# Kernel optimization log

Hardware: AMD Instinct MI355X
Metric: run time of the kernel (lower is better)

Reference implementation:

```python
import jax, jax.numpy as jnp
import numpy as np

B, C, HID, H, W = 4, 256, 128, 64, 64

def setup_inputs() -> dict:
    key = jax.random.key(0)
    k0, k1, k2, k3, k4 = jax.random.split(key, 5)
    x = jax.random.normal(k0, (B, C, H, W), dtype=jnp.float32)
    # 1x1 conv weights, no bias: [out_ch, in_ch]
    s_in = 1.0 / np.sqrt(C)
    s_hid = 1.0 / np.sqrt(HID)
    w_theta = jax.random.uniform(k1, (HID, C), jnp.float32, -s_in, s_in)
    w_phi = jax.random.uniform(k2, (HID, C), jnp.float32, -s_in, s_in)
    w_g = jax.random.uniform(k3, (HID, C), jnp.float32, -s_in, s_in)
    w_mask = jax.random.uniform(k4, (C, HID), jnp.float32, -s_hid, s_hid)
    return {"x": x, "w_theta": w_theta, "w_phi": w_phi, "w_g": w_g, "w_mask": w_mask}

def reference(x, w_theta, w_phi, w_g, w_mask):
    b, c, h, w = x.shape
    n = h * w
    xf = x.reshape(b, c, n)                      # [B,C,N]
    theta = jnp.einsum('oc,bcn->bno', w_theta, xf)  # [B,N,hid]
    phi = jnp.einsum('oc,bcn->bon', w_phi, xf)      # [B,hid,N]
    g = jnp.einsum('oc,bcn->bno', w_g, xf)          # [B,N,hid]
    scores = jnp.einsum('bnk,bkm->bnm', theta, phi)  # [B,N,N], no scale
    attn = jax.nn.softmax(scores, axis=1)            # unconventional axis=1
    out = jnp.einsum('bnm,bmo->bno', attn, g)        # [B,N,hid]
    mask = jnp.einsum('co,bno->bcn', w_mask, out).reshape(b, c, h, w)
    return x + mask
```

## Files before the change

### kernel.cpp

```cpp
#include <hip/hip_runtime.h>

#define BB 4
#define CC 256
#define HIDD 128
#define NN 4096

typedef short s8v __attribute__((ext_vector_type(8)));
typedef _Float16 h8v __attribute__((ext_vector_type(8)));
typedef float f4v __attribute__((ext_vector_type(4)));
typedef unsigned int u4v __attribute__((ext_vector_type(4)));
typedef unsigned short u16b;

static __device__ __forceinline__ float b2f(unsigned short u) {
    union { unsigned int i; float f; } v; v.i = ((unsigned int)u) << 16; return v.f;
}
static __device__ __forceinline__ unsigned short f2b(float f) {
    union { float f; unsigned int i; } v; v.f = f;
    unsigned int i = v.i;
    return (unsigned short)((i + 0x7fffu + ((i >> 16) & 1u)) >> 16);
}
static __device__ __forceinline__ u16b f2h_bits(float f) {
    union { _Float16 h; u16b u; } v; v.h = (_Float16)f; return v.u;
}
static __device__ __forceinline__ unsigned int cvt_pk_bf16(float lo, float hi) {
    unsigned int r;
    asm("v_cvt_pk_bf16_f32 %0, %1, %2" : "=v"(r) : "v"(lo), "v"(hi));
    return r;
}

__device__ __forceinline__ int swz(int k, int rc, int CB) {
    return (((k >> 5) * CB + (rc >> 4)) * 64 + ((k >> 3) & 3) * 16 + (rc & 15)) * 8 + (k & 7);
}
__device__ __forceinline__ int gswz(int m, int o) {
    int kb = m >> 5, mm = m & 31;
    int qs = (mm >> 2) & 3;
    int js = ((mm >> 4) & 1) * 4 + (mm & 3);
    return ((kb * 8 + (o >> 4)) * 64 + qs * 16 + (o & 15)) * 8 + js;
}

__global__ __launch_bounds__(256) void prep_kernel(
    const float* __restrict__ wt, const float* __restrict__ wp,
    const float* __restrict__ wg, const float* __restrict__ wm,
    u16b* __restrict__ wF, u16b* __restrict__ wmB)
{
    int t = blockIdx.x * 256 + threadIdx.x;
    wF[t]         = f2h_bits(wt[t]);
    wF[32768 + t] = f2h_bits(wp[t]);
    wF[65536 + t] = f2h_bits(wg[t]);
    wmB[t]        = f2b(wm[t]);
}

__global__ __launch_bounds__(256) void proj_kernel(
    const float* __restrict__ x, const u16b* __restrict__ wF,
    u16b* __restrict__ thetaF, u16b* __restrict__ phiF, u16b* __restrict__ gB)
{
    int wave = blockIdx.x * 4 + (threadIdx.x >> 6);
    int lane = threadIdx.x & 63;
    int l15 = lane & 15, q = lane >> 4;
    int b = wave >> 9;
    int rem = wave & 511;
    int ntile = rem >> 1;
    int half = rem & 1;
    int n0 = ntile << 4;
    const float* xb = x + (size_t)b * CC * NN;

    f4v acc[3][4];
#pragma unroll
    for (int m = 0; m < 3; m++)
#pragma unroll
        for (int i = 0; i < 4; i++) acc[m][i] = (f4v){0.f, 0.f, 0.f, 0.f};

    float xv[8];
    {
        const float* xp = xb + (size_t)(q * 8) * NN + n0 + l15;
#pragma unroll
        for (int j = 0; j < 8; j++) xv[j] = xp[(size_t)j * NN];
    }

    for (int kc = 0; kc < 8; kc++) {
        int c0 = kc * 32;
        float xn[8];
        if (kc < 7) {
            const float* xp = xb + (size_t)(c0 + 32 + q * 8) * NN + n0 + l15;
#pragma unroll
            for (int j = 0; j < 8; j++) xn[j] = xp[(size_t)j * NN];
        }
        h8v bx;
#pragma unroll
        for (int j = 0; j < 8; j++) bx[j] = (_Float16)xv[j];
#pragma unroll
        for (int mat = 0; mat < 3; mat++) {
#pragma unroll
            for (int otl = 0; otl < 4; otl++) {
                int ot = half * 4 + otl;
                const h8v* ap = reinterpret_cast<const h8v*>(
                    wF + mat * 32768 + (ot * 16 + l15) * CC + c0 + q * 8);
                acc[mat][otl] = __builtin_amdgcn_mfma_f32_16x16x32_f16(*ap, bx, acc[mat][otl], 0, 0, 0);
            }
        }
        if (kc < 7) {
#pragma unroll
            for (int j = 0; j < 8; j++) xv[j] = xn[j];
        }
    }

    size_t boff = (size_t)b * (NN * HIDD);
#pragma unroll
    for (int otl = 0; otl < 4; otl++) {
#pragma unroll
        for (int r = 0; r < 4; r++) {
            int o = (half * 4 + otl) * 16 + q * 4 + r;
            int n = n0 + l15;
            int offTP = swz(o, n, NN / 16);
            thetaF[boff + offTP] = f2h_bits(acc[0][otl][r]);
            phiF[boff + offTP]   = f2h_bits(acc[1][otl][r]);
            gB[boff + gswz(n, o)] = f2b(acc[2][otl][r]);
        }
    }
}

__global__ __launch_bounds__(256, 2) void stats_kernel(
    const u16b* __restrict__ thetaF, const u16b* __restrict__ phiF,
    float* __restrict__ Lraw)
{
    int xcd = blockIdx.x & 7;
    int inner = blockIdx.x >> 3;
    int b = xcd >> 1;
    int su = (xcd & 1) * 128 + inner;
    int w = threadIdx.x >> 6;
    int wu = su * 4 + w;
    int mg = wu >> 4;
    int ns = wu & 15;
    int lane = threadIdx.x & 63;

    size_t boff = (size_t)b * (NN * HIDD);
    const u16b* thF = thetaF + boff;
    const u16b* phF = phiF + boff;

    h8v pB[4][4];
#pragma unroll
    for (int mt = 0; mt < 4; mt++)
#pragma unroll
        for (int kb = 0; kb < 4; kb++)
            pB[mt][kb] = *reinterpret_cast<const h8v*>(phF + ((kb * 256 + (mg * 4 + mt)) * 64 + lane) * 8);

    float Lp[4];
#pragma unroll
    for (int i = 0; i < 4; i++) Lp[i] = 0.f;

    for (int i = 0; i < 16; i++) {
        int ntile = ns * 16 + i;
        h8v tA[4];
#pragma unroll
        for (int kb = 0; kb < 4; kb++)
            tA[kb] = *reinterpret_cast<const h8v*>(thF + ((kb * 256 + ntile) * 64 + lane) * 8);
#pragma unroll
        for (int mt = 0; mt < 4; mt++) {
            f4v s = (f4v){0.f, 0.f, 0.f, 0.f};
#pragma unroll
            for (int kb = 0; kb < 4; kb++)
                s = __builtin_amdgcn_mfma_f32_16x16x32_f16(tA[kb], pB[mt][kb], s, 0, 0, 0);
            Lp[mt] += (__expf(s[0]) + __expf(s[1])) + (__expf(s[2]) + __expf(s[3]));
        }
    }
#pragma unroll
    for (int mt = 0; mt < 4; mt++) {
        float v = Lp[mt];
        v += __shfl_xor(v, 16);
        v += __shfl_xor(v, 32);
        if (lane < 16) atomicAdd(&Lraw[b * NN + (mg * 4 + mt) * 16 + lane], v);
    }
}

__global__ __launch_bounds__(256) void rescale_kernel(
    u16b* __restrict__ gB, const float* __restrict__ Lraw)
{
    int t = blockIdx.x * 256 + threadIdx.x;
    int flat0 = t * 8;
    int b = flat0 >> 19;
    int rem = flat0 & ((NN * HIDD) - 1);
    int kb = rem >> 12;
    int lane = (rem >> 3) & 63;
    int qs = lane >> 4;
    int mbase = kb * 32 + qs * 4;
    const float* Lp = Lraw + b * NN + mbase;
    u16b* gp = gB + flat0;
    s8v g = *reinterpret_cast<const s8v*>(gp);
    s8v o;
#pragma unroll
    for (int j = 0; j < 8; j++) {
        float v = b2f((unsigned short)g[j]) / Lp[((j >> 2) << 4) + (j & 3)];
        o[j] = (short)f2b(v);
    }
    *reinterpret_cast<s8v*>(gp) = o;
}

__global__ __launch_bounds__(256, 2) void attn_kernel(
    const u16b* __restrict__ thetaF, const u16b* __restrict__ phiF,
    const u16b* __restrict__ gB, float* __restrict__ outAcc)
{
    int xcd = blockIdx.x & 7;
    int inner = blockIdx.x >> 3;
    int combo = xcd * 4 + (inner & 3);
    int b = combo >> 3;
    int ms = combo & 7;
    int ng = inner >> 2;
    int w = threadIdx.x >> 6;
    int lane = threadIdx.x & 63;
    int l15 = lane & 15, q = lane >> 4;
    int ntile0 = ng * 8 + w * 2;

    size_t boff = (size_t)b * (NN * HIDD);
    const u16b* thF = thetaF + boff;
    const u16b* phF = phiF + boff;
    const u16b* gp = gB + boff;

    h8v tB[2][4];
#pragma unroll
    for (int nt = 0; nt < 2; nt++)
#pragma unroll
        for (int kb = 0; kb < 4; kb++)
            tB[nt][kb] = *reinterpret_cast<const h8v*>(thF + ((kb * 256 + ntile0 + nt) * 64 + lane) * 8);

    f4v acc[2][8];
#pragma unroll
    for (int nt = 0; nt < 2; nt++)
#pragma unroll
        for (int i = 0; i < 8; i++) acc[nt][i] = (f4v){0.f, 0.f, 0.f, 0.f};

    for (int mt = 0; mt < 16; mt++) {
        int m0 = ms * 512 + mt * 32;
        s8v pf[2];
#pragma unroll
        for (int h = 0; h < 2; h++) {
            int mtile = (m0 >> 4) + h;
            h8v pA[4];
#pragma unroll
            for (int kb = 0; kb < 4; kb++)
                pA[kb] = *reinterpret_cast<const h8v*>(phF + ((kb * 256 + mtile) * 64 + lane) * 8);
#pragma unroll
            for (int nt = 0; nt < 2; nt++) {
                f4v s = (f4v){0.f, 0.f, 0.f, 0.f};
#pragma unroll
                for (int kb = 0; kb < 4; kb++)
                    s = __builtin_amdgcn_mfma_f32_16x16x32_f16(pA[kb], tB[nt][kb], s, 0, 0, 0);
#pragma unroll
                for (int r = 0; r < 4; r++)
                    pf[nt][h * 4 + r] = (short)f2b(__expf(s[r]));
            }
        }
        int kb2 = m0 >> 5;
#pragma unroll
        for (int ot = 0; ot < 8; ot++) {
            s8v gf = *reinterpret_cast<const s8v*>(gp + ((kb2 * 8 + ot) * 64 + lane) * 8);
#pragma unroll
            for (int nt = 0; nt < 2; nt++)
                acc[nt][ot] = __builtin_amdgcn_mfma_f32_16x16x32_bf16(pf[nt], gf, acc[nt][ot], 0, 0, 0);
        }
    }

    float* oa = outAcc + (size_t)b * (NN * HIDD);
#pragma unroll
    for (int nt = 0; nt < 2; nt++) {
        int n_base = (ntile0 + nt) * 16;
#pragma unroll
        for (int ot = 0; ot < 8; ot++) {
#pragma unroll
            for (int r = 0; r < 4; r++) {
                int n = n_base + q * 4 + r;
                int o = ot * 16 + l15;
                atomicAdd(&oa[swz(o, n, NN / 16)], acc[nt][ot][r]);
            }
        }
    }
}

__global__ __launch_bounds__(256, 4) void spass_kernel(
    const u16b* __restrict__ thetaF, const u16b* __restrict__ phiF,
    u16b* __restrict__ P, float* __restrict__ Lpart)
{
    int xcd = blockIdx.x & 7;
    int inner = blockIdx.x >> 3;
    int combo = xcd * 8 + (inner & 7);
    int b = combo >> 4;
    int ms = combo & 15;
    int ng = inner >> 3;
    int w = threadIdx.x >> 6;
    int lane = threadIdx.x & 63;
    int l15 = lane & 15, q = lane >> 4;
    int ntile0 = ng * 8 + w * 2;

    size_t boff = (size_t)b * (NN * HIDD);
    const u16b* thF = thetaF + boff;
    const u16b* phF = phiF + boff;
    u16b* Pb = P + (size_t)b * NN * NN;

    __shared__ float Lacc3[4 * 256 * 5];

    h8v tB[2][4];
#pragma unroll
    for (int nt = 0; nt < 2; nt++)
#pragma unroll
        for (int kb = 0; kb < 4; kb++)
            tB[nt][kb] = *reinterpret_cast<const h8v*>(thF + ((kb * 256 + ntile0 + nt) * 64 + lane) * 8);

    int ph = ng & 7;
    h8v pA[4];
    {
        int mtile = ms * 16 + ph * 2;
#pragma unroll
        for (int kb = 0; kb < 4; kb++)
            pA[kb] = *reinterpret_cast<const h8v*>(phF + ((kb * 256 + mtile) * 64 + lane) * 8);
    }

    for (int i2 = 0; i2 < 8; i2++) {
        int mtr = (i2 + ph) & 7;
        unsigned int p000, p001, p010, p011;
        unsigned int p100, p101, p110, p111;
#pragma unroll
        for (int h = 0; h < 2; h++) {
            int nmtile = (h == 0) ? (ms * 16 + mtr * 2 + 1)
                                  : (ms * 16 + (((i2 + 1 + ph) & 7)) * 2);
            h8v pAN[4];
#pragma unroll
            for (int kb = 0; kb < 4; kb++)
                pAN[kb] = *reinterpret_cast<const h8v*>(phF + ((kb * 256 + nmtile) * 64 + lane) * 8);
            f4v s0 = (f4v){0.f, 0.f, 0.f, 0.f};
            f4v s1 = (f4v){0.f, 0.f, 0.f, 0.f};
#pragma unroll
            for (int kb = 0; kb < 4; kb++) {
                s0 = __builtin_amdgcn_mfma_f32_16x16x32_f16(pA[kb], tB[0][kb], s0, 0, 0, 0);
                s1 = __builtin_amdgcn_mfma_f32_16x16x32_f16(pA[kb], tB[1][kb], s1, 0, 0, 0);
            }
            float ev0[4], ev1[4];
#pragma unroll
            for (int r = 0; r < 4; r++) {
                ev0[r] = __expf(s0[r]);
                ev1[r] = __expf(s1[r]);
            }
            if (h == 0) {
                p000 = cvt_pk_bf16(ev0[0], ev0[1]);
                p001 = cvt_pk_bf16(ev0[2], ev0[3]);
                p100 = cvt_pk_bf16(ev1[0], ev1[1]);
                p101 = cvt_pk_bf16(ev1[2], ev1[3]);
            } else {
                p010 = cvt_pk_bf16(ev0[0], ev0[1]);
                p011 = cvt_pk_bf16(ev0[2], ev0[3]);
                p110 = cvt_pk_bf16(ev1[0], ev1[1]);
                p111 = cvt_pk_bf16(ev1[2], ev1[3]);
            }
            int tloc = mtr * 32 + h * 16 + q * 4;
            float cs[4];
#pragma unroll
            for (int r = 0; r < 4; r++) {
                cs[r] = ev0[r] + ev1[r];
                cs[r] += __shfl_xor(cs[r], 1);
                cs[r] += __shfl_xor(cs[r], 2);
            }
            if ((l15 & 3) == 0) {
#pragma unroll
                for (int r = 0; r < 4; r++)
                    Lacc3[(w * 256 + tloc + r) * 5 + (l15 >> 2)] = cs[r];
            }
#pragma unroll
            for (int kb = 0; kb < 4; kb++) pA[kb] = pAN[kb];
        }
        int kb2 = ms * 8 + mtr;
        u4v pf0 = (u4v){p000, p001, p010, p011};
        u4v pf1 = (u4v){p100, p101, p110, p111};
        *reinterpret_cast<u4v*>(Pb + ((size_t)(kb2 * 256 + ntile0 + 0) * 64 + lane) * 8) = pf0;
        *reinterpret_cast<u4v*>(Pb + ((size_t)(kb2 * 256 + ntile0 + 1) * 64 + lane) * 8) = pf1;
    }
    __syncthreads();
    {
        int t = threadIdx.x;
        float s = 0.f;
#pragma unroll
        for (int w4 = 0; w4 < 4; w4++) {
            float ps = 0.f;
#pragma unroll
            for (int j = 0; j < 4; j++)
                ps += Lacc3[(w4 * 256 + t) * 5 + j];
            s += ps;
        }
        Lpart[((size_t)(combo * 32 + ng)) * 256 + t] = s;
    }
}

__global__ __launch_bounds__(256) void lrescale_kernel(
    u16b* __restrict__ gB, const float* __restrict__ Lpart)
{
    int t = blockIdx.x;
    int b = t >> 8;
    int kb = (t & 255) >> 1;
    int combo = b * 16 + (kb >> 3);
    int mlbase = (kb & 7) * 32;
    __shared__ float sLp[32][9];
    __shared__ float sL[32];
    int ti = threadIdx.x;
    {
        int mi = ti & 31;
        int ngp = ti >> 5;
        int qs = mi >> 3, h = (mi >> 2) & 1, r = mi & 3;
        int ml = mlbase + qs * 4 + h * 16 + r;
        const float* base = Lpart + ((size_t)(combo * 32 + ngp * 4)) * 256 + ml;
        sLp[mi][ngp] = (base[0] + base[256]) + (base[512] + base[768]);
    }
    __syncthreads();
    if (ti < 32) {
        float s = 0.f;
#pragma unroll
        for (int k = 0; k < 8; k++) s += sLp[ti][k];
        sL[ti] = s;
    }
    __syncthreads();
    size_t flat0 = (size_t)b * (NN * HIDD) + (size_t)(t & 255) * 2048 + (size_t)ti * 8;
    int lane = ti & 63;
    int qs = lane >> 4;
    u16b* gp = gB + flat0;
    s8v g = *reinterpret_cast<const s8v*>(gp);
    s8v o;
#pragma unroll
    for (int j = 0; j < 8; j++) {
        int mi = qs * 8 + ((j >> 2) << 2) + (j & 3);
        float v = b2f((unsigned short)g[j]) / sL[mi];
        o[j] = (short)f2b(v);
    }
    *reinterpret_cast<s8v*>(gp) = o;
}

__global__ __launch_bounds__(256, 3) void pv_kernel(
    const u16b* __restrict__ P, const u16b* __restrict__ gB, u16b* __restrict__ pvPart)
{
    int xcd = blockIdx.x & 7;
    int inner = blockIdx.x >> 3;
    int combo = xcd * 2 + (inner & 1);
    int b = combo >> 2;
    int ms = combo & 3;
    int ng = inner >> 1;
    int w = threadIdx.x >> 6;
    int lane = threadIdx.x & 63;
    int l15 = lane & 15, q = lane >> 4;
    int ntile = ng * 4 + w;

    const u16b* Pb = P + (size_t)b * NN * NN;
    const u16b* gp = gB + (size_t)b * (NN * HIDD);

    __shared__ __align__(16) u16b gS[4 * 8 * 512];

    f4v acc[8];
#pragma unroll
    for (int i = 0; i < 8; i++) acc[i] = (f4v){0.f, 0.f, 0.f, 0.f};

    int ph = ng & 31;
    int ot0 = w * 2;

    s8v p0, p1, p2, p3;

#define PV_KB2(it) (ms * 32 + (((it) + ph) & 31))
#define PV_ISSUE(it, sl, preg) do {                                              \
    int kb2_ = PV_KB2(it);                                                       \
    const u16b* s0_ = gp + (((size_t)(kb2_ * 8 + ot0) * 64 + lane) * 8);         \
    __builtin_amdgcn_global_load_lds(                                            \
        (const __attribute__((address_space(1))) unsigned int*)s0_,              \
        (__attribute__((address_space(3))) unsigned int*)(&gS[((sl) * 8 + ot0) * 512]), \
        16, 0, 0);                                                               \
    __builtin_amdgcn_global_load_lds(                                            \
        (const __attribute__((address_space(1))) unsigned int*)(s0_ + 512),      \
        (__attribute__((address_space(3))) unsigned int*)(&gS[((sl) * 8 + ot0 + 1) * 512]), \
        16, 0, 0);                                                               \
    preg = *reinterpret_cast<const s8v*>(                                        \
        Pb + ((size_t)(kb2_ * 256 + ntile) * 64 + lane) * 8);                    \
} while (0)

#define PV_STEP(it, sl, pcons, pnew) do {                                        \
    PV_ISSUE((it) + 2, ((sl) + 2) & 3, pnew);                                    \
    __builtin_amdgcn_sched_barrier(0);                                           \
    asm volatile("s_waitcnt vmcnt(6)" ::: "memory");                             \
    __builtin_amdgcn_sched_barrier(0);                                           \
    __builtin_amdgcn_s_barrier();                                                \
    __builtin_amdgcn_sched_barrier(0);                                           \
    const s8v* gs_ = reinterpret_cast<const s8v*>(gS) + (sl) * 512 + lane;       \
    s8v g0_ = gs_[0];   s8v g1_ = gs_[64];  s8v g2_ = gs_[128]; s8v g3_ = gs_[192]; \
    s8v g4_ = gs_[256]; s8v g5_ = gs_[320]; s8v g6_ = gs_[384]; s8v g7_ = gs_[448]; \
    acc[0] = __builtin_amdgcn_mfma_f32_16x16x32_bf16(pcons, g0_, acc[0], 0, 0, 0); \
    acc[1] = __builtin_amdgcn_mfma_f32_16x16x32_bf16(pcons, g1_, acc[1], 0, 0, 0); \
    acc[2] = __builtin_amdgcn_mfma_f32_16x16x32_bf16(pcons, g2_, acc[2], 0, 0, 0); \
    acc[3] = __builtin_amdgcn_mfma_f32_16x16x32_bf16(pcons, g3_, acc[3], 0, 0, 0); \
    acc[4] = __builtin_amdgcn_mfma_f32_16x16x32_bf16(pcons, g4_, acc[4], 0, 0, 0); \
    acc[5] = __builtin_amdgcn_mfma_f32_16x16x32_bf16(pcons, g5_, acc[5], 0, 0, 0); \
    acc[6] = __builtin_amdgcn_mfma_f32_16x16x32_bf16(pcons, g6_, acc[6], 0, 0, 0); \
    acc[7] = __builtin_amdgcn_mfma_f32_16x16x32_bf16(pcons, g7_, acc[7], 0, 0, 0); \
} while (0)

    PV_ISSUE(0, 0, p0);
    PV_ISSUE(1, 1, p1);

    for (int i8 = 0; i8 < 32; i8 += 4) {
        PV_STEP(i8 + 0, 0, p0, p2);
        PV_STEP(i8 + 1, 1, p1, p3);
        PV_STEP(i8 + 2, 2, p2, p0);
        PV_STEP(i8 + 3, 3, p3, p1);
    }
#undef PV_STEP
#undef PV_ISSUE
#undef PV_KB2

    u16b* pp = pvPart + (size_t)ms * ((size_t)BB * NN * HIDD) + (size_t)b * (NN * HIDD);
    int n_base = ntile * 16;
#pragma unroll
    for (int ot = 0; ot < 8; ot++) {
#pragma unroll
        for (int r = 0; r < 4; r++) {
            int n = n_base + q * 4 + r;
            int o = ot * 16 + l15;
            pp[swz(o, n, NN / 16)] = f2b(acc[ot][r]);
        }
    }
}

__global__ __launch_bounds__(256) void final_big_kernel(
    const float* __restrict__ x, const u16b* __restrict__ wmB,
    const u16b* __restrict__ pvPart, float* __restrict__ y)
{
    int wave = blockIdx.x * 4 + (threadIdx.x >> 6);
    int lane = threadIdx.x & 63;
    int l15 = lane & 15, q = lane >> 4;
    int b = wave >> 10;
    int rem = wave & 1023;
    int ctile = rem >> 6;
    int n64 = rem & 63;
    const size_t pstride = (size_t)BB * NN * HIDD;
    const u16b* pb = pvPart + (size_t)b * (NN * HIDD);
    const float* xb = x + (size_t)b * CC * NN;
    float* yb = y + (size_t)b * CC * NN;
    int c0 = ctile * 16;

    s8v aB[4];
#pragma unroll
    for (int kb = 0; kb < 4; kb++)
        aB[kb] = *reinterpret_cast<const s8v*>(wmB + (c0 + l15) * HIDD + kb * 32 + q * 8);

#pragma unroll
    for (int nt = 0; nt < 4; nt++) {
        int ntile = n64 * 4 + nt;
        f4v acc = (f4v){0.f, 0.f, 0.f, 0.f};
#pragma unroll
        for (int kb = 0; kb < 4; kb++) {
            size_t fo = ((size_t)(kb * 256 + ntile) * 64 + lane) * 8;
            s8v v0 = *reinterpret_cast<const s8v*>(pb + 0 * pstride + fo);
            s8v v1 = *reinterpret_cast<const s8v*>(pb + 1 * pstride + fo);
            s8v v2 = *reinterpret_cast<const s8v*>(pb + 2 * pstride + fo);
            s8v v3 = *reinterpret_cast<const s8v*>(pb + 3 * pstride + fo);
            s8v bv;
#pragma unroll
            for (int j = 0; j < 8; j++) {
                float s = (b2f((unsigned short)v0[j]) + b2f((unsigned short)v1[j]))
                        + (b2f((unsigned short)v2[j]) + b2f((unsigned short)v3[j]));
                bv[j] = (short)f2b(s);
            }
            acc = __builtin_amdgcn_mfma_f32_16x16x32_bf16(aB[kb], bv, acc, 0, 0, 0);
        }
#pragma unroll
        for (int r = 0; r < 4; r++) {
            int c = c0 + q * 4 + r;
            int n = ntile * 16 + l15;
            size_t idx = (size_t)c * NN + n;
            yb[idx] = xb[idx] + acc[r];
        }
    }
}

__global__ __launch_bounds__(256) void final_kernel(
    const float* __restrict__ x, const u16b* __restrict__ wmB,
    const float* __restrict__ outAcc, float* __restrict__ y)
{
    int wave = blockIdx.x * 4 + (threadIdx.x >> 6);
    int lane = threadIdx.x & 63;
    int l15 = lane & 15, q = lane >> 4;
    int b = wave >> 10;
    int rem = wave & 1023;
    int ctile = rem >> 6;
    int n64 = rem & 63;
    const float* oa = outAcc + (size_t)b * (NN * HIDD);
    const float* xb = x + (size_t)b * CC * NN;
    float* yb = y + (size_t)b * CC * NN;
    int c0 = ctile * 16;

    s8v aB[4];
#pragma unroll
    for (int kb = 0; kb < 4; kb++)
        aB[kb] = *reinterpret_cast<const s8v*>(wmB + (c0 + l15) * HIDD + kb * 32 + q * 8);

#pragma unroll
    for (int nt = 0; nt < 4; nt++) {
        int ntile = n64 * 4 + nt;
        f4v acc = (f4v){0.f, 0.f, 0.f, 0.f};
#pragma unroll
        for (int kb = 0; kb < 4; kb++) {
            const float* bp = oa + ((size_t)(kb * 256 + ntile) * 64 + lane) * 8;
            f4v b0 = *reinterpret_cast<const f4v*>(bp);
            f4v b1 = *reinterpret_cast<const f4v*>(bp + 4);
            s8v bv;
#pragma unroll
            for (int j = 0; j < 4; j++) {
                bv[j]     = (short)f2b(b0[j]);
                bv[j + 4] = (short)f2b(b1[j]);
            }
            acc = __builtin_amdgcn_mfma_f32_16x16x32_bf16(aB[kb], bv, acc, 0, 0, 0);
        }
#pragma unroll
        for (int r = 0; r < 4; r++) {
            int c = c0 + q * 4 + r;
            int n = ntile * 16 + l15;
            size_t idx = (size_t)c * NN + n;
            yb[idx] = xb[idx] + acc[r];
        }
    }
}

extern "C" void kernel_launch(void* const* d_in, const int* in_sizes, int n_in,
                              void* d_out, int out_size, void* d_ws, size_t ws_size,
                              hipStream_t stream)
{
    (void)in_sizes; (void)n_in; (void)out_size;
    const float* x  = (const float*)d_in[0];
    const float* wt = (const float*)d_in[1];
    const float* wp = (const float*)d_in[2];
    const float* wg = (const float*)d_in[3];
    const float* wm = (const float*)d_in[4];
    float* y = (float*)d_out;

    char* ws = (char*)d_ws;
    const size_t MB = 1 << 20;
    u16b* thetaF = (u16b*)(ws + 0 * MB);
    u16b* phiF   = (u16b*)(ws + 4 * MB);
    u16b* pvPart = (u16b*)(ws + 0 * MB);
    u16b* gB     = (u16b*)(ws + 16 * MB);
    float* outAcc = (float*)(ws + 20 * MB);
    float* Lraw   = (float*)(ws + 28 * MB);
    char* wbase = ws + 28 * MB + (64 << 10);
    u16b* wF  = (u16b*)(wbase);
    u16b* wmB = (u16b*)(wbase + (192 << 10));
    float* Lpart = (float*)(ws + 30 * MB);
    u16b* P   = (u16b*)(ws + 32 * MB);

    const size_t need_big = 32 * MB + (size_t)BB * NN * NN * sizeof(u16b);
    const bool big = ws_size >= need_big;

    hipLaunchKernelGGL(prep_kernel, dim3(128), dim3(256), 0, stream,
                       wt, wp, wg, wm, wF, wmB);
    hipLaunchKernelGGL(proj_kernel, dim3(512), dim3(256), 0, stream,
                       x, wF, thetaF, phiF, gB);

    if (big) {
        hipLaunchKernelGGL(spass_kernel,    dim3(2048), dim3(256), 0, stream,
                           thetaF, phiF, P, Lpart);
        hipLaunchKernelGGL(lrescale_kernel, dim3(1024), dim3(256), 0, stream, gB, Lpart);
        hipLaunchKernelGGL(pv_kernel,       dim3(1024), dim3(256), 0, stream, P, gB, pvPart);
        hipLaunchKernelGGL(final_big_kernel, dim3(1024), dim3(256), 0, stream,
                           x, wmB, pvPart, y);
    } else {
        hipMemsetAsync(Lraw, 0, (size_t)BB * NN * sizeof(float), stream);
        hipMemsetAsync(outAcc, 0, (size_t)BB * NN * HIDD * sizeof(float), stream);
        hipLaunchKernelGGL(stats_kernel,   dim3(1024), dim3(256), 0, stream,
                           thetaF, phiF, Lraw);
        hipLaunchKernelGGL(rescale_kernel, dim3(1024), dim3(256), 0, stream, gB, Lraw);
        hipLaunchKernelGGL(attn_kernel,    dim3(1024), dim3(256), 0, stream,
                           thetaF, phiF, gB, outAcc);
        hipLaunchKernelGGL(final_kernel,   dim3(1024), dim3(256), 0, stream,
                           x, wmB, outAcc, y);
    }
}
```

Measured before the change: 177.5 us.

## Fold log2e into phi weights, use exp2, deepen P prefetch in pv_kernel

Scales the phi projection weights by log2(e) during weight prep, so the score kernels can use exp2f in place of __expf and skip the per-element multiply. Separately, pv_kernel now prefetches the P fragment three iterations ahead instead of two, with the wait count adjusted to match. Its launch bounds are raised to 4 blocks per SM for occupancy. The deeper prefetch adds register pressure under the tighter occupancy bound. Scaling in fp16 also slightly changes the rounding of phi.

New measurement: 188.7 us. 6.3% more time.

```diff
diff --git a/kernel.cpp b/kernel.cpp
--- a/kernel.cpp
+++ b/kernel.cpp
@@ -45,7 +45,7 @@
 {
     int t = blockIdx.x * 256 + threadIdx.x;
     wF[t]         = f2h_bits(wt[t]);
-    wF[32768 + t] = f2h_bits(wp[t]);
+    wF[32768 + t] = f2h_bits(wp[t] * 1.44269504088896f);
     wF[65536 + t] = f2h_bits(wg[t]);
     wmB[t]        = f2b(wm[t]);
 }
@@ -160,7 +160,7 @@
 #pragma unroll
             for (int kb = 0; kb < 4; kb++)
                 s = __builtin_amdgcn_mfma_f32_16x16x32_f16(tA[kb], pB[mt][kb], s, 0, 0, 0);
-            Lp[mt] += (__expf(s[0]) + __expf(s[1])) + (__expf(s[2]) + __expf(s[3]));
+            Lp[mt] += (exp2f(s[0]) + exp2f(s[1])) + (exp2f(s[2]) + exp2f(s[3]));
         }
     }
 #pragma unroll
@@ -246,7 +246,7 @@
                     s = __builtin_amdgcn_mfma_f32_16x16x32_f16(pA[kb], tB[nt][kb], s, 0, 0, 0);
 #pragma unroll
                 for (int r = 0; r < 4; r++)
-                    pf[nt][h * 4 + r] = (short)f2b(__expf(s[r]));
+                    pf[nt][h * 4 + r] = (short)f2b(exp2f(s[r]));
             }
         }
         int kb2 = m0 >> 5;
@@ -335,8 +335,8 @@
             float ev0[4], ev1[4];
 #pragma unroll
             for (int r = 0; r < 4; r++) {
-                ev0[r] = __expf(s0[r]);
-                ev1[r] = __expf(s1[r]);
+                ev0[r] = exp2f(s0[r]);
+                ev1[r] = exp2f(s1[r]);
             }
             if (h == 0) {
                 p000 = cvt_pk_bf16(ev0[0], ev0[1]);
@@ -429,7 +429,7 @@
     *reinterpret_cast<s8v*>(gp) = o;
 }
 
-__global__ __launch_bounds__(256, 3) void pv_kernel(
+__global__ __launch_bounds__(256, 4) void pv_kernel(
     const u16b* __restrict__ P, const u16b* __restrict__ gB, u16b* __restrict__ pvPart)
 {
     int xcd = blockIdx.x & 7;
@@ -458,7 +458,7 @@
     s8v p0, p1, p2, p3;
 
 #define PV_KB2(it) (ms * 32 + (((it) + ph) & 31))
-#define PV_ISSUE(it, sl, preg) do {                                              \
+#define PV_G_ISSUE(it, sl) do {                                                  \
     int kb2_ = PV_KB2(it);                                                       \
     const u16b* s0_ = gp + (((size_t)(kb2_ * 8 + ot0) * 64 + lane) * 8);         \
     __builtin_amdgcn_global_load_lds(                                            \
@@ -469,14 +469,17 @@
         (const __attribute__((address_space(1))) unsigned int*)(s0_ + 512),      \
         (__attribute__((address_space(3))) unsigned int*)(&gS[((sl) * 8 + ot0 + 1) * 512]), \
         16, 0, 0);                                                               \
+} while (0)
+#define PV_P_ISSUE(it, preg) do {                                                \
     preg = *reinterpret_cast<const s8v*>(                                        \
-        Pb + ((size_t)(kb2_ * 256 + ntile) * 64 + lane) * 8);                    \
+        Pb + ((size_t)(PV_KB2(it) * 256 + ntile) * 64 + lane) * 8);              \
 } while (0)
 
-#define PV_STEP(it, sl, pcons, pnew) do {                                        \
-    PV_ISSUE((it) + 2, ((sl) + 2) & 3, pnew);                                    \
+#define PV_STEP(it, sl, pcons, pdst) do {                                        \
+    PV_G_ISSUE((it) + 2, ((sl) + 2) & 3);                                        \
+    PV_P_ISSUE((it) + 3, pdst);                                                  \
     __builtin_amdgcn_sched_barrier(0);                                           \
-    asm volatile("s_waitcnt vmcnt(6)" ::: "memory");                             \
+    asm volatile("s_waitcnt vmcnt(7)" ::: "memory");                             \
     __builtin_amdgcn_sched_barrier(0);                                           \
     __builtin_amdgcn_s_barrier();                                                \
     __builtin_amdgcn_sched_barrier(0);                                           \
@@ -493,17 +496,21 @@
     acc[7] = __builtin_amdgcn_mfma_f32_16x16x32_bf16(pcons, g7_, acc[7], 0, 0, 0); \
 } while (0)
 
-    PV_ISSUE(0, 0, p0);
-    PV_ISSUE(1, 1, p1);
+    PV_P_ISSUE(0, p0);
+    PV_G_ISSUE(0, 0);
+    PV_P_ISSUE(1, p1);
+    PV_G_ISSUE(1, 1);
+    PV_P_ISSUE(2, p2);
 
     for (int i8 = 0; i8 < 32; i8 += 4) {
-        PV_STEP(i8 + 0, 0, p0, p2);
-        PV_STEP(i8 + 1, 1, p1, p3);
-        PV_STEP(i8 + 2, 2, p2, p0);
-        PV_STEP(i8 + 3, 3, p3, p1);
+        PV_STEP(i8 + 0, 0, p0, p3);
+        PV_STEP(i8 + 1, 1, p1, p0);
+        PV_STEP(i8 + 2, 2, p2, p1);
+        PV_STEP(i8 + 3, 3, p3, p2);
     }
 #undef PV_STEP
-#undef PV_ISSUE
+#undef PV_P_ISSUE
+#undef PV_G_ISSUE
 #undef PV_KB2
 
     u16b* pp = pvPart + (size_t)ms * ((size_t)BB * NN * HIDD) + (size_t)b * (NN * HIDD);
```
